# Performance work log

Hardware: AMD Instinct MI355X
Metric: run time of the kernel (lower is better)

Reference implementation:

```python
import jax, jax.numpy as jnp
import numpy as np

B, D, TX, TY = 32, 192, 256, 1024
NEG = -1e9


def setup_inputs() -> dict:
    key = jax.random.key(0)
    k1, k2, k3, k4 = jax.random.split(key, 4)
    x = jax.random.normal(k1, (B, D, TX), jnp.float32)
    y = jax.random.normal(k2, (B, D, TY), jnp.float32)
    # ensure 1 <= x_lens <= TX <= y_lens <= TY so a monotonic path exists
    x_lens = jax.random.randint(k3, (B,), 64, TX + 1, jnp.int32)
    y_lens = jax.random.randint(k4, (B,), 512, TY + 1, jnp.int32)
    return {"x": x, "x_lens": x_lens, "y": y, "y_lens": y_lens}


def _log_prior(x, y):
    # Gaussian log-prior: factor = -0.5 everywhere, so
    # log_prior[b,t,s] = -0.5*sum_d y^2 + sum_d x*y - 0.5*sum_d x^2 + const
    ndim = x.shape[1]
    const = jnp.asarray(-0.5 * np.log(2.0 * np.pi) * ndim, x.dtype)
    y_sq = -0.5 * jnp.sum(y * y, axis=1)            # [B, TY]
    x_sq = -0.5 * jnp.sum(x * x, axis=1)            # [B, TX]
    xy = jnp.einsum('bdt,bds->bts', x, y)           # [B, TX, TY]
    return y_sq[:, None, :] + xy + x_sq[:, :, None] + const


def _maximum_path(log_prior, x_lens, y_lens):
    # Viterbi-style monotonic alignment search (Glow-TTS / VITS maximum_path).
    b, tx, ty = log_prior.shape
    xr = jnp.arange(tx)

    # --- forward DP over mel frames (columns of the (tx, ty) grid) ---
    col0 = jnp.where(xr[None, :] == 0, log_prior[:, :, 0], NEG)  # [B, TX]

    def fwd(prev, inp):
        lp_col, yi = inp                               # lp_col: [B, TX]
        v_cur = jnp.where(xr[None, :] == yi, NEG, prev)
        v_prev = jnp.concatenate(
            [jnp.full((b, 1), NEG, prev.dtype), prev[:, :-1]], axis=1)
        cur = lp_col + jnp.maximum(v_cur, v_prev)
        return cur, cur

    lp_t = jnp.moveaxis(log_prior, 2, 0)               # [TY, B, TX]
    _, cols = jax.lax.scan(fwd, col0, (lp_t[1:], jnp.arange(1, ty)))
    value = jnp.concatenate([col0[None], cols], axis=0)  # [TY, B, TX]

    # value at column y-1 (dummy at y=0, never used for the decision there)
    vprev = jnp.concatenate([value[:1], value[:-1]], axis=0)

    # --- backtrack from (x_lens-1, y_lens-1) down to y=0 ---
    def bwd(index, inp):
        yi, vpc = inp                                  # vpc: [B, TX]
        active = yi < y_lens                           # [B]
        row = jnp.where(active[:, None],
                        jax.nn.one_hot(index, tx, dtype=log_prior.dtype), 0.0)
        vm1 = jnp.take_along_axis(
            vpc, jnp.maximum(index - 1, 0)[:, None], axis=1)[:, 0]
        v0 = jnp.take_along_axis(vpc, index[:, None], axis=1)[:, 0]
        move = (index != 0) & ((index == yi) | (vm1 > v0)) & active
        return index - move.astype(index.dtype), row

    idx0 = x_lens - 1
    _, rows = jax.lax.scan(bwd, idx0, (jnp.arange(ty), vprev), reverse=True)
    return jnp.moveaxis(rows, 0, 2)                    # [B, TX, TY]


def reference(x, x_lens, y, y_lens):
    log_prior = _log_prior(x, y)
    attn = _maximum_path(log_prior, x_lens, y_lens)
    return jax.lax.stop_gradient(attn)
```

## Files before the change

kernel.cpp:

```cpp
#include <hip/hip_runtime.h>
#include <stdint.h>

#define B_  32
#define D_  192
#define TX_ 256
#define TY_ 1024
#define NEGV -1e9f
#define LPCONST ((float)(-176.43619837529715))

__global__ __launch_bounds__(256) void k0_sq(const float* __restrict__ x,
                                             const float* __restrict__ y,
                                             float* __restrict__ xsq,
                                             float* __restrict__ ysq) {
    int gid = blockIdx.x * 256 + threadIdx.x;
    if (gid < B_ * TX_) {
        int b = gid >> 8, t = gid & 255;
        const float* p = x + (size_t)b * D_ * TX_ + t;
        float s = 0.f;
        #pragma unroll 8
        for (int d = 0; d < D_; ++d) { float v = p[(size_t)d * TX_]; s += v * v; }
        xsq[gid] = -0.5f * s;
    } else {
        int g = gid - B_ * TX_;
        int b = g >> 10, t = g & 1023;
        const float* p = y + (size_t)b * D_ * TY_ + t;
        float s = 0.f;
        #pragma unroll 8
        for (int d = 0; d < D_; ++d) { float v = p[(size_t)d * TY_]; s += v * v; }
        ysq[g] = -0.5f * s;
    }
}

#define BT 128
#define BS 128
#define BK 32
__global__ __launch_bounds__(256) void k1_gemm(const float* __restrict__ x,
                                               const float* __restrict__ y,
                                               const float* __restrict__ xsq,
                                               const float* __restrict__ ysq,
                                               float* __restrict__ lp) {
    __shared__ float xs[BK][BT];
    __shared__ float ys[BK][BS];
    const int id = blockIdx.x;
    const int r  = id & 7;
    const int g  = id >> 3;
    const int b  = r + 8 * (g >> 4);
    const int sub = g & 15;
    const int t0 = (sub >> 3) * BT;
    const int s0 = (sub & 7) * BS;
    const int tid = threadIdx.x;
    const int ti = tid & 15;
    const int si = tid >> 4;

    float acc[8][8];
    #pragma unroll
    for (int i = 0; i < 8; ++i)
        #pragma unroll
        for (int j = 0; j < 8; ++j) acc[i][j] = 0.f;

    const float* xg = x + (size_t)b * D_ * TX_ + t0;
    const float* yg = y + (size_t)b * D_ * TY_ + s0;

    for (int k0 = 0; k0 < D_; k0 += BK) {
        #pragma unroll
        for (int i = 0; i < 4; ++i) {
            int f = tid + i * 256;
            int row = f >> 5;
            int col = (f & 31) * 4;
            float4 v = *(const float4*)(xg + (size_t)(k0 + row) * TX_ + col);
            *(float4*)&xs[row][col] = v;
            float4 w = *(const float4*)(yg + (size_t)(k0 + row) * TY_ + col);
            *(float4*)&ys[row][col] = w;
        }
        __syncthreads();
        #pragma unroll
        for (int k = 0; k < BK; ++k) {
            float xr[8], yr[8];
            *(float4*)&xr[0] = *(float4*)&xs[k][ti * 8];
            *(float4*)&xr[4] = *(float4*)&xs[k][ti * 8 + 4];
            *(float4*)&yr[0] = *(float4*)&ys[k][si * 8];
            *(float4*)&yr[4] = *(float4*)&ys[k][si * 8 + 4];
            #pragma unroll
            for (int i = 0; i < 8; ++i)
                #pragma unroll
                for (int j = 0; j < 8; ++j) acc[i][j] += xr[i] * yr[j];
        }
        __syncthreads();
    }

    float xq[8], yq[8];
    *(float4*)&xq[0] = *(const float4*)(xsq + b * TX_ + t0 + ti * 8);
    *(float4*)&xq[4] = *(const float4*)(xsq + b * TX_ + t0 + ti * 8 + 4);
    *(float4*)&yq[0] = *(const float4*)(ysq + b * TY_ + s0 + si * 8);
    *(float4*)&yq[4] = *(const float4*)(ysq + b * TY_ + s0 + si * 8 + 4);

    #pragma unroll
    for (int js = 0; js < 8; ++js) {
        float* op = lp + (size_t)(b * TY_ + s0 + si * 8 + js) * TX_ + t0 + ti * 8;
        float o[8];
        #pragma unroll
        for (int it = 0; it < 8; ++it) {
            float v = yq[js] + acc[it][js];
            v = v + xq[it];
            o[it] = v + LPCONST;
        }
        *(float4*)op       = *(float4*)&o[0];
        *(float4*)(op + 4) = *(float4*)&o[4];
    }
}

__global__ __launch_bounds__(256) void k15_warm(const float* __restrict__ lp,
                                                const int* __restrict__ xlens) {
    const int p  = blockIdx.x;
    const int r  = p & 7;
    const int b  = r + 8 * ((p >> 3) & 3);
    const int c0 = (p >> 5) * 128;
    const int xlen = xlens[b];
    const int tid = threadIdx.x;
    const int e = (tid & 63) * 4;
    const float* base = lp + (size_t)b * TY_ * TX_;
    float acc = 0.f;
    if (e < xlen) {
        #pragma unroll 8
        for (int it = 0; it < 32; ++it) {
            int col = c0 + it * 4 + (tid >> 6);
            float4 v = *(const float4*)(base + (size_t)col * TX_ + e);
            acc += v.x + v.y + v.z + v.w;
        }
    }
    asm volatile("" :: "v"(acc));
}

__device__ __forceinline__ float wshr1(float v) {
    int r = __builtin_amdgcn_update_dpp(0, __float_as_int(v),
                                        0x138, 0xF, 0xF, false);
    return __int_as_float(r);
}

#define PROC(s, fv, PRE) {                                              \
    unsigned int sbit = 1u << ((s) & 31);                               \
    bool e0 = false, e1 = false, e2 = false, e3 = false;                \
    if (PRE) { e0 = (tt0 == (s));     e1 = (tt0 + 1 == (s));            \
               e2 = (tt0 + 2 == (s)); e3 = (tt0 + 3 == (s)); }          \
    if ((l != 0) && (e0 || (shv > p0))) rw0 |= sbit;                    \
    if (e1 || (p0 > p1)) rw1 |= sbit;                                   \
    if (e2 || (p1 > p2)) rw2 |= sbit;                                   \
    if (e3 || (p2 > p3)) rw3 |= sbit;                                   \
    float c3 = (fv).w + fmaxf(e3 ? NEGV : p3, p2);                      \
    float nsh = wshr1(c3);                                              \
    float c2 = (fv).z + fmaxf(e2 ? NEGV : p2, p1);                      \
    float c1 = (fv).y + fmaxf(e1 ? NEGV : p1, p0);                      \
    float c0 = (fv).x + fmaxf(e0 ? NEGV : p0, (l == 0) ? NEGV : shv);   \
    p0 = c0; p1 = c1; p2 = c2; p3 = c3; shv = nsh;                      \
}

#define FLUSH(w) { RB[tt0][w] = rw0; RB[tt0 + 1][w] = rw1;              \
                   RB[tt0 + 2][w] = rw2; RB[tt0 + 3][w] = rw3;          \
                   rw0 = rw1 = rw2 = rw3 = 0; }

__global__ __launch_bounds__(64, 1) void k2_dp(const float* __restrict__ lp,
                                               const int* __restrict__ xlens,
                                               const int* __restrict__ ylens,
                                               unsigned char* __restrict__ path) {
    __shared__ unsigned int RB[TX_][33];
    __shared__ unsigned int PTw[TY_ / 4];
    unsigned char* PT = (unsigned char*)PTw;

    const int b = blockIdx.x;
    const int l = threadIdx.x;
    const int xlen = xlens[b];
    const int ylen = ylens[b];
    const int send = (ylen + 31) & ~31;
    const int tt0 = l * 4;
    const int rowsel = (tt0 < xlen) ? tt0 : ((xlen - 1) & ~15);
    const float* base = lp + (size_t)b * TY_ * TX_ + rowsel;

#define LDCOL(s) (*(const float4*)(base + (size_t)(((s) < TY_) ? (s) : (TY_ - 1)) * TX_))

    float4 g[16];
    #pragma unroll
    for (int i = 0; i < 16; ++i) g[i] = LDCOL(i);

    float p0, p1, p2, p3, shv;
    unsigned int rw0 = 0, rw1 = 0, rw2 = 0, rw3 = 0;

    p0 = (l == 0) ? g[0].x : NEGV;
    p1 = NEGV; p2 = NEGV; p3 = NEGV;
    shv = NEGV;
    g[0] = LDCOL(16);

    #pragma unroll
    for (int j = 1; j < 16; ++j) { PROC(j, g[j], true) g[j] = LDCOL(16 + j); }

    #pragma unroll 1
    for (int sb = 16; sb < 256; sb += 16) {
        #pragma unroll
        for (int j = 0; j < 16; ++j) { PROC(sb + j, g[j], true) g[j] = LDCOL(sb + 16 + j); }
        if (((sb + 15) & 31) == 31) FLUSH((sb + 15) >> 5)
    }
    #pragma unroll 1
    for (int sb = 256; sb < send; sb += 16) {
        #pragma unroll
        for (int j = 0; j < 16; ++j) { PROC(sb + j, g[j], false) g[j] = LDCOL(sb + 16 + j); }
        if (((sb + 15) & 31) == 31) FLUSH((sb + 15) >> 5)
    }
    __syncthreads();

    if (l == 0) {
        int idx = xlen - 1;
        int yi = ylen - 1;
        int w = yi >> 5;
        unsigned int cur = RB[idx][w];
        unsigned int below = (idx > 0) ? RB[idx - 1][w] : 0u;
        while (yi >= 0) {
            unsigned int m = cur & (0xFFFFFFFFu >> (31 - (yi & 31)));
            if (m) {
                int hb = 31 - __clz(m);
                int lo = (w << 5) + hb;
                for (int q = lo; q <= yi; ++q) PT[q] = (unsigned char)idx;
                --idx;
                cur = below;
                below = (idx > 0) ? RB[idx - 1][w] : 0u;
                yi = lo - 1;
                if (yi >= 0 && (yi >> 5) < w) {
                    w = yi >> 5;
                    cur = RB[idx][w];
                    below = (idx > 0) ? RB[idx - 1][w] : 0u;
                }
            } else {
                int lo = w << 5;
                for (int q = lo; q <= yi; ++q) PT[q] = (unsigned char)idx;
                yi = lo - 1;
                if (yi >= 0) {
                    --w;
                    cur = RB[idx][w];
                    below = (idx > 0) ? RB[idx - 1][w] : 0u;
                }
            }
        }
    }
    __syncthreads();
    {
        unsigned int* pd = (unsigned int*)(path + b * TY_);
        #pragma unroll
        for (int k = 0; k < 4; ++k) pd[l + k * 64] = PTw[l + k * 64];
    }
}

__global__ __launch_bounds__(256) void k3_out(const unsigned char* __restrict__ path,
                                              const int* __restrict__ ylens,
                                              float* __restrict__ out) {
    int F = blockIdx.x * 256 + threadIdx.x;
    int yi = (F & 255) * 4;
    int t  = (F >> 8) & 255;
    int b  = F >> 16;
    int ylen = ylens[b];
    unsigned int pw = *(const unsigned int*)(path + b * TY_ + yi);
    float4 v;
    v.x = (((pw      ) & 255u) == (unsigned)t && yi     < ylen) ? 1.f : 0.f;
    v.y = (((pw >>  8) & 255u) == (unsigned)t && yi + 1 < ylen) ? 1.f : 0.f;
    v.z = (((pw >> 16) & 255u) == (unsigned)t && yi + 2 < ylen) ? 1.f : 0.f;
    v.w = (((pw >> 24) & 255u) == (unsigned)t && yi + 3 < ylen) ? 1.f : 0.f;
    ((float4*)out)[F] = v;
}

extern "C" void kernel_launch(void* const* d_in, const int* in_sizes, int n_in,
                              void* d_out, int out_size, void* d_ws, size_t ws_size,
                              hipStream_t stream) {
    const float* x  = (const float*)d_in[0];
    const int*   xl = (const int*)d_in[1];
    const float* y  = (const float*)d_in[2];
    const int*   yl = (const int*)d_in[3];
    float* out = (float*)d_out;

    char* ws = (char*)d_ws;
    float* xsq = (float*)ws;
    float* ysq = (float*)(ws + 32 * 1024);
    unsigned char* path = (unsigned char*)(ws + 160 * 1024);

    float* lp = out;

    k0_sq   <<<160, 256, 0, stream>>>(x, y, xsq, ysq);
    k1_gemm <<<512, 256, 0, stream>>>(x, y, xsq, ysq, lp);
    k15_warm<<<256, 256, 0, stream>>>(lp, xl);
    k2_dp   <<<B_, 64, 0, stream>>>(lp, xl, yl, path);
    k3_out  <<<(B_ * TX_ * TY_ / 4) / 256, 256, 0, stream>>>(path, yl, out);
}
```

Measured before the change: 192.8 us.

## Stripe DP rows across lanes to remove serial intra-lane dependency chain

The Viterbi forward DP now assigns rows l, l+64, l+128, l+192 to each lane instead of four contiguous rows, so the four per-lane updates are independent and each takes its predecessor from a DPP shift or rotate of the previous column. This shortens the per-column critical path, which before was a serial chain through p0..p3 plus a cross-lane shift. In exchange, each column needs four scalar strided loads instead of one float4 load, and more DPP ops per step.

```diff
diff --git a/kernel.cpp b/kernel.cpp
--- a/kernel.cpp
+++ b/kernel.cpp
@@ -136,27 +136,11 @@
                                         0x138, 0xF, 0xF, false);
     return __int_as_float(r);
 }
-
-#define PROC(s, fv, PRE) {                                              \
-    unsigned int sbit = 1u << ((s) & 31);                               \
-    bool e0 = false, e1 = false, e2 = false, e3 = false;                \
-    if (PRE) { e0 = (tt0 == (s));     e1 = (tt0 + 1 == (s));            \
-               e2 = (tt0 + 2 == (s)); e3 = (tt0 + 3 == (s)); }          \
-    if ((l != 0) && (e0 || (shv > p0))) rw0 |= sbit;                    \
-    if (e1 || (p0 > p1)) rw1 |= sbit;                                   \
-    if (e2 || (p1 > p2)) rw2 |= sbit;                                   \
-    if (e3 || (p2 > p3)) rw3 |= sbit;                                   \
-    float c3 = (fv).w + fmaxf(e3 ? NEGV : p3, p2);                      \
-    float nsh = wshr1(c3);                                              \
-    float c2 = (fv).z + fmaxf(e2 ? NEGV : p2, p1);                      \
-    float c1 = (fv).y + fmaxf(e1 ? NEGV : p1, p0);                      \
-    float c0 = (fv).x + fmaxf(e0 ? NEGV : p0, (l == 0) ? NEGV : shv);   \
-    p0 = c0; p1 = c1; p2 = c2; p3 = c3; shv = nsh;                      \
-}
-
-#define FLUSH(w) { RB[tt0][w] = rw0; RB[tt0 + 1][w] = rw1;              \
-                   RB[tt0 + 2][w] = rw2; RB[tt0 + 3][w] = rw3;          \
-                   rw0 = rw1 = rw2 = rw3 = 0; }
+__device__ __forceinline__ float wror1(float v) {
+    int r = __builtin_amdgcn_update_dpp(0, __float_as_int(v),
+                                        0x13C, 0xF, 0xF, false);
+    return __int_as_float(r);
+}
 
 __global__ __launch_bounds__(64, 1) void k2_dp(const float* __restrict__ lp,
                                                const int* __restrict__ xlens,
@@ -171,37 +155,64 @@
     const int xlen = xlens[b];
     const int ylen = ylens[b];
     const int send = (ylen + 31) & ~31;
-    const int tt0 = l * 4;
-    const int rowsel = (tt0 < xlen) ? tt0 : ((xlen - 1) & ~15);
-    const float* base = lp + (size_t)b * TY_ * TX_ + rowsel;
-
-#define LDCOL(s) (*(const float4*)(base + (size_t)(((s) < TY_) ? (s) : (TY_ - 1)) * TX_))
-
-    float4 g[16];
-    #pragma unroll
-    for (int i = 0; i < 16; ++i) g[i] = LDCOL(i);
-
-    float p0, p1, p2, p3, shv;
+    const float* lpb = lp + (size_t)b * TY_ * TX_;
+    const float* base0 = lpb + l;
+    const float* base1 = lpb + ((l + 64  < xlen) ? (l + 64)  : (xlen - 1));
+    const float* base2 = lpb + ((l + 128 < xlen) ? (l + 128) : (xlen - 1));
+    const float* base3 = lpb + ((l + 192 < xlen) ? (l + 192) : (xlen - 1));
+
+#define LD4(j, s) { int sc = ((s) < TY_) ? (s) : (TY_ - 1);             \
+    g0[j] = base0[(size_t)sc * TX_]; g1[j] = base1[(size_t)sc * TX_];   \
+    g2[j] = base2[(size_t)sc * TX_]; g3[j] = base3[(size_t)sc * TX_]; }
+
+#define PROCS(s, j, PRE) {                                              \
+    unsigned int sbit = 1u << ((s) & 31);                               \
+    float a0 = wshr1(v0), a1 = wshr1(v1), a2 = wshr1(v2), a3 = wshr1(v3); \
+    float q0 = wror1(v0), q1 = wror1(v1), q2 = wror1(v2);               \
+    float s1v = (l == 0) ? q0 : a1;                                     \
+    float s2v = (l == 0) ? q1 : a2;                                     \
+    float s3v = (l == 0) ? q2 : a3;                                     \
+    bool e0 = false, e1 = false, e2 = false, e3 = false;                \
+    if (PRE) { e0 = (l == (s));        e1 = (l + 64 == (s));            \
+               e2 = (l + 128 == (s));  e3 = (l + 192 == (s)); }         \
+    if ((l != 0) && (e0 || (a0  > v0))) rw0 |= sbit;                    \
+    if (e1 || (s1v > v1)) rw1 |= sbit;                                  \
+    if (e2 || (s2v > v2)) rw2 |= sbit;                                  \
+    if (e3 || (s3v > v3)) rw3 |= sbit;                                  \
+    v0 = g0[j] + fmaxf(e0 ? NEGV : v0, (l == 0) ? NEGV : a0);           \
+    v1 = g1[j] + fmaxf(e1 ? NEGV : v1, s1v);                            \
+    v2 = g2[j] + fmaxf(e2 ? NEGV : v2, s2v);                            \
+    v3 = g3[j] + fmaxf(e3 ? NEGV : v3, s3v);                            \
+}
+
+#define FLUSH(w) { RB[l][w] = rw0; RB[l + 64][w] = rw1;                 \
+                   RB[l + 128][w] = rw2; RB[l + 192][w] = rw3;          \
+                   rw0 = rw1 = rw2 = rw3 = 0; }
+
+    float g0[16], g1[16], g2[16], g3[16];
+    #pragma unroll
+    for (int i = 0; i < 16; ++i) LD4(i, i)
+
+    float v0, v1, v2, v3;
     unsigned int rw0 = 0, rw1 = 0, rw2 = 0, rw3 = 0;
 
-    p0 = (l == 0) ? g[0].x : NEGV;
-    p1 = NEGV; p2 = NEGV; p3 = NEGV;
-    shv = NEGV;
-    g[0] = LDCOL(16);
-
-    #pragma unroll
-    for (int j = 1; j < 16; ++j) { PROC(j, g[j], true) g[j] = LDCOL(16 + j); }
+    v0 = (l == 0) ? g0[0] : NEGV;
+    v1 = NEGV; v2 = NEGV; v3 = NEGV;
+    LD4(0, 16)
+
+    #pragma unroll
+    for (int j = 1; j < 16; ++j) { PROCS(j, j, true) LD4(j, 16 + j) }
 
     #pragma unroll 1
     for (int sb = 16; sb < 256; sb += 16) {
         #pragma unroll
-        for (int j = 0; j < 16; ++j) { PROC(sb + j, g[j], true) g[j] = LDCOL(sb + 16 + j); }
+        for (int j = 0; j < 16; ++j) { PROCS(sb + j, j, true) LD4(j, sb + 16 + j) }
         if (((sb + 15) & 31) == 31) FLUSH((sb + 15) >> 5)
     }
     #pragma unroll 1
     for (int sb = 256; sb < send; sb += 16) {
         #pragma unroll
-        for (int j = 0; j < 16; ++j) { PROC(sb + j, g[j], false) g[j] = LDCOL(sb + 16 + j); }
+        for (int j = 0; j < 16; ++j) { PROCS(sb + j, j, false) LD4(j, sb + 16 + j) }
         if (((sb + 15) & 31) == 31) FLUSH((sb + 15) >> 5)
     }
     __syncthreads();
```

Result: slower. 229.8 us (+19.2%).
